# Performance work log

Measured on AMD Instinct MI355X. Metric: run time of the kernel, lower is better.

## Reference

```python
import jax, jax.numpy as jnp
import numpy as np
from functools import partial

WIDTH = 2560
LRU = 2560
HEADS = 8
DCONV = 4
B = 4
L = 2048


def setup_inputs() -> dict:
    key = jax.random.key(0)
    ks = jax.random.split(key, 16)
    bw = LRU // HEADS
    x = jax.random.normal(ks[0], (B, L, WIDTH), dtype=jnp.float32)
    segment_pos = jnp.broadcast_to(jnp.arange(L, dtype=jnp.int32), (B, L))
    # indices of the last DCONV frames of the left-padded conv input (length L+DCONV-1)
    base = (jnp.arange(DCONV, dtype=jnp.int32) + (L - 1))
    conv_idx = jnp.broadcast_to(base, (B, LRU, DCONV))
    s = 0.02
    return {
        "x": x,
        "segment_pos": segment_pos,
        "conv_idx": conv_idx,
        "Wx": jax.random.normal(ks[1], (LRU, WIDTH), jnp.float32) * s,
        "bx": jax.random.normal(ks[2], (LRU,), jnp.float32) * s,
        "Wy": jax.random.normal(ks[3], (LRU, WIDTH), jnp.float32) * s,
        "conv_w": jax.random.normal(ks[4], (LRU, DCONV), jnp.float32) * s,  # depthwise kernel
        "conv_b": jax.random.normal(ks[5], (LRU,), jnp.float32) * s,
        "gx_w": jax.random.normal(ks[6], (HEADS, bw, bw), jnp.float32) * s,
        "gx_b": jax.random.normal(ks[7], (HEADS, bw), jnp.float32) * s,
        "ga_w": jax.random.normal(ks[8], (HEADS, bw, bw), jnp.float32) * s,
        "ga_b": jax.random.normal(ks[9], (HEADS, bw), jnp.float32) * s,
        "a_param": jax.random.normal(ks[10], (LRU,), jnp.float32),
        "y_bias": jax.random.normal(ks[11], (1, 1, LRU), jnp.float32) * s,
        "Wout": jax.random.normal(ks[12], (WIDTH, LRU), jnp.float32) * s,
        "bout": jax.random.normal(ks[13], (WIDTH,), jnp.float32) * s,
    }


def _block_diag(x, w):
    # x: [B,L,(h*i)], w: [h,i,j] -> [B,L,(h*j)]
    b, l, _ = x.shape
    h, bw, _ = w.shape
    xb = x.reshape(b, l, h, bw)
    y = jnp.einsum('blhi,hij->blhj', xb, w)
    return y.reshape(b, l, h * bw)


def _scan_op(c1, c2):
    a1, b1 = c1
    a2, b2 = c2
    return (a1 * a2, a2 * b1 + b2)


def reference(x, segment_pos, conv_idx, Wx, bx, Wy, conv_w, conv_b,
              gx_w, gx_b, ga_w, ga_b, a_param, y_bias, Wout, bout):
    dc = conv_w.shape[1]
    seqlen = x.shape[1]

    y = jnp.einsum('bld,ed->ble', x, Wy)                 # linear_y (no bias)
    xl = jnp.einsum('bld,ed->ble', x, Wx) + bx           # linear_x

    # causal depthwise conv1d, padding dc-1 on the left, keep first seqlen
    xpad = jnp.pad(xl, ((0, 0), (dc - 1, 0), (0, 0)))    # [B, L+dc-1, LRU]
    xc = conv_b + sum(conv_w[:, k] * xpad[:, k:k + seqlen, :] for k in range(dc))

    # conv_state: gather of padded (channels-first) input at conv_idx
    conv_state = jnp.take_along_axis(xpad.transpose(0, 2, 1), conv_idx.astype(jnp.int32), axis=2)

    gx = _block_diag(xc, gx_w)  # fuse_bias=True: bias added inside rg_lru
    ga = _block_diag(xc, ga_w)

    # rg_lru_ref
    reset = (segment_pos == 0).astype(x.dtype)[..., None]        # [B,L,1]
    gate_x = jax.nn.sigmoid(gx + gx_b.reshape(-1))
    gate_a = jax.nn.sigmoid(ga + ga_b.reshape(-1))
    c = -8.0 * jax.nn.softplus(a_param)
    log_a = c * gate_a
    a = jnp.exp(log_a) * (1.0 - reset)
    multiplier = jnp.sqrt(1.0 - jnp.exp(2.0 * log_a))
    multiplier = reset + (1.0 - reset) * multiplier
    normalized_x = xc * gate_x * multiplier

    _, h = jax.lax.associative_scan(_scan_op, (a, normalized_x), axis=1)
    last_h = h[:, -1]

    out = h * jax.nn.gelu(y + y_bias, approximate=False)
    out = jnp.einsum('ble,de->bld', out, Wout) + bout    # linear_out
    return out, conv_state, last_h
```

## Files before the change

kernel.cpp:

```cpp
#include <hip/hip_runtime.h>
#include <hip/hip_bf16.h>

#define WIDTH_ 2560
#define LRU_   2560
#define HEADS_ 8
#define BW_    320
#define DCONV_ 4
#define BB     4
#define LL     2048
#define MROWS  (BB*LL)
#define NCH    32
#define CLEN   (LL/NCH)

typedef unsigned short ushort_t;
typedef __attribute__((ext_vector_type(8))) short short8;
typedef __attribute__((ext_vector_type(4))) float f32x4;

__device__ __forceinline__ unsigned short f2bf(float f) {
  union { float f; unsigned u; } v; v.f = f;
  unsigned r = v.u + 0x7fffu + ((v.u >> 16) & 1u);
  return (unsigned short)(r >> 16);
}
__device__ __forceinline__ float bf2f(unsigned short h) {
  union { unsigned u; float f; } v; v.u = ((unsigned)h) << 16;
  return v.f;
}
__device__ __forceinline__ void async_load16(const void* g, void* l) {
  __builtin_amdgcn_global_load_lds(
      (const __attribute__((address_space(1))) unsigned*)g,
      (__attribute__((address_space(3))) unsigned*)l, 16, 0, 0);
}
__device__ __forceinline__ float sigmoidf_(float x) {
  return 1.f / (1.f + __expf(-x));
}
__device__ __forceinline__ size_t pkaddr(int e, int m, int PL) {
  return ((size_t)(e >> 3) * PL + m) * 8 + (e & 7);
}

__global__ void tp_pack(const float* __restrict__ src, ushort_t* __restrict__ dst,
                        int R, int C, int PL, int RO) {
  __shared__ float tile[64][65];
  const int r0 = blockIdx.x * 64, c0 = blockIdx.y * 64;
  const int t = threadIdx.x;
#pragma unroll
  for (int it = 0; it < 4; ++it) {
    int row = it * 16 + (t >> 4);
    int col = (t & 15) * 4;
    *(float4*)&tile[row][col] = *(const float4*)&src[(size_t)(r0 + row) * C + c0 + col];
  }
  __syncthreads();
#pragma unroll
  for (int it = 0; it < 2; ++it) {
    int c8 = it * 4 + (t >> 6);
    int m  = t & 63;
    ushort_t o[8];
#pragma unroll
    for (int j = 0; j < 8; ++j) o[j] = f2bf(tile[m][c8 * 8 + j]);
    *(short8*)&dst[((size_t)(c0 / 8 + c8) * PL + RO + r0 + m) * 8] = *(short8*)o;
  }
}

__global__ void gw_pack2(const float* __restrict__ gxw, const float* __restrict__ gaw,
                         ushort_t* __restrict__ dst, int n_) {
  int i = blockIdx.x * blockDim.x + threadIdx.x;
  if (i >= 2 * n_) return;
  const float* w = (i < n_) ? gxw : gaw;
  int RO = (i < n_) ? 0 : BW_;
  int j = (i < n_) ? i : i - n_;
  int n = j % BW_;
  int k = (j / BW_) % BW_;
  int h = j / (BW_ * BW_);
  dst[((size_t)(h * 40 + (k >> 3)) * 640 + RO + n) * 8 + (k & 7)] =
      f2bf(w[((size_t)h * BW_ + k) * BW_ + n]);
}

__global__ void ctab_kernel(const float* __restrict__ apar, float* __restrict__ ctab) {
  int e = blockIdx.x * blockDim.x + threadIdx.x;
  if (e >= LRU_) return;
  float ap = apar[e];
  float sp = (ap > 15.f) ? ap : log1pf(expf(ap));
  ctab[e] = -8.f * sp;
}


#define STG_A(KT, H, BUF) do { \
  _Pragma("unroll") for (int u_ = 0; u_ < 2; ++u_) \
    async_load16(Ach + aoff[u_] + (size_t)(KT) * aKt + (H) * 2048, \
                 smem + ((BUF) * 2 + (H)) * 16384 + ldst[u_]); } while (0)
#define STG_B(KT, PART, BUF) do { \
  _Pragma("unroll") for (int u_ = (PART) ? 2 : 0; u_ < ((PART) ? NF : 2); ++u_) \
    async_load16(Bch + boff[u_] + (size_t)(KT) * bKt, \
                 smem + 65536 + (BUF) * BREG + bldst[u_]); } while (0)

#define PHASE(BUF, Q, STAGE_STMT, VMN) do { \
  __builtin_amdgcn_sched_barrier(0); \
  const char* Ah_ = smem + ((BUF) * 2 + wr) * 16384; \
  const char* Bh_ = smem + 65536 + (BUF) * BREG; \
  if ((Q) == 0) { \
    _Pragma("unroll") for (int nf = 0; nf < NF; ++nf) \
      _Pragma("unroll") for (int s = 0; s < 2; ++s) \
        bfr[nf][s] = *(const short8*)(Bh_ + (((s * 4 + l4) * BN) + wc * (BN / 4) + nf * 16 + l15) * 16); \
  } \
  short8 a_[2][2]; \
  _Pragma("unroll") for (int mm = 0; mm < 2; ++mm) \
    _Pragma("unroll") for (int s = 0; s < 2; ++s) \
      a_[mm][s] = *(const short8*)(Ah_ + ((s * 4 + l4) * 128 + ((Q) * 2 + mm) * 16 + l15) * 16); \
  STAGE_STMT; \
  __builtin_amdgcn_sched_barrier(0); \
  __builtin_amdgcn_s_barrier(); \
  asm volatile("s_waitcnt lgkmcnt(0)" ::: "memory"); \
  __builtin_amdgcn_sched_barrier(0); \
  __builtin_amdgcn_s_setprio(1); \
  _Pragma("unroll") for (int mm = 0; mm < 2; ++mm) \
    _Pragma("unroll") for (int nf = 0; nf < NF; ++nf) \
      _Pragma("unroll") for (int s = 0; s < 2; ++s) \
        acc[(Q) * 2 + mm][nf] = __builtin_amdgcn_mfma_f32_16x16x32_bf16( \
            a_[mm][s], bfr[nf][s], acc[(Q) * 2 + mm][nf], 0, 0, 0); \
  __builtin_amdgcn_s_setprio(0); \
  if ((VMN) == 5)      asm volatile("s_waitcnt vmcnt(5)" ::: "memory"); \
  else if ((VMN) == 4) asm volatile("s_waitcnt vmcnt(4)" ::: "memory"); \
  else if ((VMN) == 0) asm volatile("s_waitcnt vmcnt(0)" ::: "memory"); \
  __builtin_amdgcn_sched_barrier(0); \
  __builtin_amdgcn_s_barrier(); \
} while (0)

template<int EPI, int BN>
__global__ __launch_bounds__(512, 2)
void gemm_pk(const ushort_t* __restrict__ A,
             const ushort_t* __restrict__ B, int NPL,
             void* __restrict__ C0, void* __restrict__ C1,
             const float* __restrict__ bias) {
  constexpr int NF = BN / 64;
  constexpr int BREG = BN * 128;
  __shared__ char smem[65536 + 2 * BREG];
  const int tid = threadIdx.x;
  const int lane = tid & 63, w = tid >> 6;
  const int wr = w >> 2, wc = w & 3;
  const int l15 = lane & 15, l4 = lane >> 4;

  const int nblk = gridDim.x;
  const int TN = nblk >> 5;
  const int x8 = blockIdx.x & 7, c = blockIdx.x >> 3;
  const int tm = (x8 * 4 + c / TN) * 256;
  const int tn = (c % TN) * BN;

  const char* Ach = (const char*)A;
  const char* Bch = (const char*)B;
  const size_t aKt = (size_t)8 * MROWS * 16;
  const size_t bKt = (size_t)8 * NPL * 16;

  size_t aoff[2]; int ldst[2];
#pragma unroll
  for (int u = 0; u < 2; ++u) {
    int lb = (u * 512 + tid) * 16;
    int slot = lb >> 11, m = (lb >> 4) & 127;
    aoff[u] = ((size_t)slot * MROWS + tm + m) * 16;
    ldst[u] = lb;
  }
  size_t boff[NF]; int bldst[NF];
#pragma unroll
  for (int u = 0; u < NF; ++u) {
    int lb = (u * 512 + tid) * 16;
    int slot = lb / (BN * 16), n = (lb - slot * (BN * 16)) >> 4;
    boff[u] = ((size_t)slot * NPL + tn + n) * 16;
    bldst[u] = lb;
  }

  f32x4 acc[8][NF] = {};
  short8 bfr[NF][2];

  STG_B(0, 0, 0); STG_B(0, 1, 0);
  STG_A(0, 0, 0); STG_A(0, 1, 0);
  STG_B(1, 0, 1); STG_B(1, 1, 1);
  if (NF == 5) asm volatile("s_waitcnt vmcnt(5)" ::: "memory");
  else         asm volatile("s_waitcnt vmcnt(4)" ::: "memory");
  __builtin_amdgcn_sched_barrier(0);
  __builtin_amdgcn_s_barrier();

#pragma unroll 1
  for (int i = 0; i < 20; ++i) {
    const int k1 = 2 * i + 1, k2 = 2 * i + 2, k3 = 2 * i + 3;
    const bool v2 = (k2 < 40), v3 = (k3 < 40);
    PHASE(0, 0, STG_A(k1, 0, 1), -1);
    PHASE(0, 1, STG_A(k1, 1, 1), -1);
    PHASE(0, 2, if (v2) STG_B(k2, 0, 0), -1);
    PHASE(0, 3, if (v2) STG_B(k2, 1, 0), (v2 ? NF : 0));
    PHASE(1, 0, if (v2) STG_A(k2, 0, 0), -1);
    PHASE(1, 1, if (v2) STG_A(k2, 1, 0), -1);
    PHASE(1, 2, if (v3) STG_B(k3, 0, 1), -1);
    PHASE(1, 3, if (v3) STG_B(k3, 1, 1), (v3 ? NF : (v2 ? 0 : -1)));
  }

  const int crow0 = tm + wr * 128 + l4 * 4;
  const int ccol0 = tn + wc * (BN / 4) + l15;
#pragma unroll
  for (int m = 0; m < 8; ++m)
#pragma unroll
    for (int n = 0; n < NF; ++n) {
      const int col = ccol0 + n * 16;
#pragma unroll
      for (int r = 0; r < 4; ++r) {
        const int row = crow0 + m * 16 + r;
        float v = acc[m][n][r];
        if (EPI == 0) {
          ((float*)C0)[(size_t)row * 2560 + col] = v + bias[col];
        } else {
          if (col < 2560)
            ((ushort_t*)C0)[pkaddr(col, row, MROWS)] = f2bf(v + bias[col]);
          else
            ((ushort_t*)C1)[pkaddr(col - 2560, row, MROWS)] = f2bf(v);
        }
      }
    }
}

__global__ __launch_bounds__(256, 2)
void gate_gemm(const ushort_t* __restrict__ A,
               const ushort_t* __restrict__ Bw,
               ushort_t* __restrict__ GX,
               ushort_t* __restrict__ AAo,
               const float* __restrict__ gxb, const float* __restrict__ gab,
               const float* __restrict__ ctab, const int* __restrict__ seg) {
  constexpr int BM = 128, NF = 2;
  __shared__ char smem[24576];
  const int tid = threadIdx.x;
  const int w = tid >> 6, lane = tid & 63;
  const int wr = w >> 1, wc = w & 1;
  const int l15 = lane & 15, l4 = lane >> 4;

  const int bid = blockIdx.x;
  const int x8 = bid & 7;
  const int s = bid >> 3;
  const int member = s % 10;
  const int g = (s / 10) * 8 + x8;
  const int tm = (g & 63) * BM;
  const int z = g >> 6;
  const int tn = member * 64;

  const char* aS[2]; int lda_[2];
#pragma unroll
  for (int u = 0; u < 2; ++u) {
    int lb = (u * 256 + tid) * 16;
    int slot = lb >> 11, m = (lb >> 4) & 127;
    aS[u] = (const char*)A + ((size_t)(z * 40 + slot) * MROWS + tm + m) * 16;
    lda_[u] = lb;
  }
  const char* bS; int ldb_;
  {
    int lb = tid * 16;
    int slot = lb >> 10, n = (lb >> 4) & 63;
    bS = (const char*)Bw + ((size_t)(z * 40 + slot) * 640 + tn + n) * 16;
    ldb_ = 8192 + lb;
  }
  const size_t aStep = (size_t)4 * MROWS * 16;
  const size_t bStep = (size_t)4 * 640 * 16;

#define GSTG(KT, BUF) do { \
  _Pragma("unroll") for (int u_ = 0; u_ < 2; ++u_) \
    async_load16(aS[u_] + (size_t)(KT) * aStep, smem + (BUF) * 12288 + lda_[u_]); \
  async_load16(bS + (size_t)(KT) * bStep, smem + (BUF) * 12288 + ldb_); \
} while (0)

  f32x4 acc[4][NF] = {};
  const int aRd = l4 * 2048 + (wr * 64 + l15) * 16;
  const int bRd = 8192 + l4 * 1024 + (wc * 32 + l15) * 16;

  GSTG(0, 0);
#pragma unroll 1
  for (int kt = 0; kt < 10; ++kt) {
    const int p = kt & 1;
    if (kt < 9) {
      GSTG(kt + 1, p ^ 1);
      asm volatile("s_waitcnt vmcnt(3)" ::: "memory");
    } else {
      asm volatile("s_waitcnt vmcnt(0)" ::: "memory");
    }
    __builtin_amdgcn_sched_barrier(0);
    __builtin_amdgcn_s_barrier();
    const char* buf = smem + p * 12288;
    short8 af[4], bfr[NF];
#pragma unroll
    for (int mf = 0; mf < 4; ++mf)
      af[mf] = *(const short8*)(buf + aRd + mf * 256);
#pragma unroll
    for (int nf = 0; nf < NF; ++nf)
      bfr[nf] = *(const short8*)(buf + bRd + nf * 256);
#pragma unroll
    for (int mf = 0; mf < 4; ++mf)
#pragma unroll
      for (int nf = 0; nf < NF; ++nf)
        acc[mf][nf] = __builtin_amdgcn_mfma_f32_16x16x32_bf16(af[mf], bfr[nf], acc[mf][nf], 0, 0, 0);
    __builtin_amdgcn_sched_barrier(0);
    __builtin_amdgcn_s_barrier();
  }
#undef GSTG

  const int crow0 = tm + wr * 64 + l4 * 4;
  const int ccol0 = tn + wc * 32 + l15;
#pragma unroll
  for (int mf = 0; mf < 4; ++mf) {
#pragma unroll
    for (int nf = 0; nf < NF; ++nf) {
      const int cih = ccol0 + nf * 16;
#pragma unroll
      for (int r = 0; r < 4; ++r) {
        const int row = crow0 + mf * 16 + r;
        if (cih < BW_) {
          const int gc = z * BW_ + cih;
          float v = acc[mf][nf][r] + gxb[gc];
          float xc = bf2f(A[pkaddr(gc, row, MROWS)]);
          GX[pkaddr(gc, row, MROWS)] = f2bf(xc * sigmoidf_(v));
        } else {
          const int gc = z * BW_ + cih - BW_;
          float v = acc[mf][nf][r] + gab[gc];
          float la = ctab[gc] * sigmoidf_(v);
          float av = (seg[row] == 0) ? 0.f : expf(la);
          AAo[pkaddr(gc, row, MROWS)] = f2bf(av);
        }
      }
    }
  }
}

__global__ void conv_pk(const ushort_t* __restrict__ xl, const float* __restrict__ convw,
                        const float* __restrict__ convb, ushort_t* __restrict__ xc) {
  int i = blockIdx.x * blockDim.x + threadIdx.x;
  if (i >= 320 * MROWS) return;
  int m = i % MROWS;
  int p = i / MROWS;
  int t = m % LL;
  const ushort_t* pl = xl + (size_t)p * MROWS * 8;
  short8 v0 = {}, v1 = {}, v2 = {}, v3;
  v3 = *(const short8*)(pl + (size_t)m * 8);
  if (t >= 1) v2 = *(const short8*)(pl + (size_t)(m - 1) * 8);
  if (t >= 2) v1 = *(const short8*)(pl + (size_t)(m - 2) * 8);
  if (t >= 3) v0 = *(const short8*)(pl + (size_t)(m - 3) * 8);
  ushort_t o[8];
#pragma unroll
  for (int u = 0; u < 8; ++u) {
    int e = p * 8 + u;
    float4 wv = ((const float4*)convw)[e];
    float acc = convb[e];
    acc += wv.x * bf2f((ushort_t)v0[u]);
    acc += wv.y * bf2f((ushort_t)v1[u]);
    acc += wv.z * bf2f((ushort_t)v2[u]);
    acc += wv.w * bf2f((ushort_t)v3[u]);
    o[u] = f2bf(acc);
  }
  *(short8*)(xc + (size_t)p * MROWS * 8 + (size_t)m * 8) = *(short8*)o;
}

__global__ void conv_state_kernel(const ushort_t* __restrict__ xl, const int* __restrict__ cidx,
                                  float* __restrict__ cs) {
  int i = blockIdx.x * blockDim.x + threadIdx.x;
  if (i >= BB * LRU_ * DCONV_) return;
  int e = (i / DCONV_) % LRU_;
  int b = i / (DCONV_ * LRU_);
  int idx = cidx[i];
  int ts = idx - (DCONV_ - 1);
  float v = 0.f;
  if (ts >= 0 && ts < LL) v = bf2f(xl[pkaddr(e, b * LL + ts, MROWS)]);
  cs[i] = v;
}

__global__ void scanA(const ushort_t* __restrict__ AA, const ushort_t* __restrict__ GX,
                      float* __restrict__ cA, float* __restrict__ cH) {
  int i = blockIdx.x * blockDim.x + threadIdx.x;
  if (i >= BB * NCH * LRU_) return;
  int e = i % LRU_;
  int c = (i / LRU_) % NCH;
  int b = i / (LRU_ * NCH);
  float Ap = 1.f, h = 0.f;
  size_t base = pkaddr(e, b * LL + c * CLEN, MROWS);
  for (int t = 0; t < CLEN; ++t) {
    size_t j = base + (size_t)t * 8;
    float a = bf2f(AA[j]);
    float nx = bf2f(GX[j]) * sqrtf(fmaxf(0.f, 1.f - a * a));
    Ap *= a;
    h = a * h + nx;
  }
  cA[i] = Ap; cH[i] = h;
}

__global__ void scanB(const float* __restrict__ cA, const float* __restrict__ cH,
                      float* __restrict__ hInit) {
  int i = blockIdx.x * blockDim.x + threadIdx.x;
  if (i >= BB * LRU_) return;
  int e = i % LRU_;
  int b = i / LRU_;
  float h = 0.f;
  for (int c = 0; c < NCH; ++c) {
    size_t j = ((size_t)b * NCH + c) * LRU_ + e;
    hInit[j] = h;
    h = cA[j] * h + cH[j];
  }
}

__global__ void scanC(const ushort_t* __restrict__ AA, const ushort_t* __restrict__ GXpre,
                      const float* __restrict__ hInit, const ushort_t* __restrict__ ybf,
                      const float* __restrict__ ybias, float* __restrict__ lastH) {
  int i = blockIdx.x * blockDim.x + threadIdx.x;
  if (i >= BB * NCH * LRU_) return;
  int e = i % LRU_;
  int c = (i / LRU_) % NCH;
  int b = i / (LRU_ * NCH);
  float h = hInit[i];
  float yb = ybias[e];
  ushort_t* pre = (ushort_t*)GXpre;
  size_t base = pkaddr(e, b * LL + c * CLEN, MROWS);
  for (int t = 0; t < CLEN; ++t) {
    size_t j = base + (size_t)t * 8;
    float a = bf2f(AA[j]);
    float nx = bf2f(GXpre[j]) * sqrtf(fmaxf(0.f, 1.f - a * a));
    h = a * h + nx;
    float yv = bf2f(ybf[j]) + yb;
    float g = 0.5f * yv * (1.f + erff(yv * 0.70710678118f));
    pre[j] = f2bf(h * g);
  }
  if (c == NCH - 1) lastH[(size_t)b * LRU_ + e] = h;
}

extern "C" void kernel_launch(void* const* d_in, const int* in_sizes, int n_in,
                              void* d_out, int out_size, void* d_ws, size_t ws_size,
                              hipStream_t stream) {
  const float* x     = (const float*)d_in[0];
  const int*   seg   = (const int*)d_in[1];
  const int*   cidx  = (const int*)d_in[2];
  const float* Wx    = (const float*)d_in[3];
  const float* bx    = (const float*)d_in[4];
  const float* Wy    = (const float*)d_in[5];
  const float* convw = (const float*)d_in[6];
  const float* convb = (const float*)d_in[7];
  const float* gxw   = (const float*)d_in[8];
  const float* gxb   = (const float*)d_in[9];
  const float* gaw   = (const float*)d_in[10];
  const float* gab   = (const float*)d_in[11];
  const float* apar  = (const float*)d_in[12];
  const float* ybias = (const float*)d_in[13];
  const float* Wout  = (const float*)d_in[14];
  const float* bout  = (const float*)d_in[15];

  float* out    = (float*)d_out;
  float* cs_out = out + (size_t)MROWS * WIDTH_;
  float* lh_out = cs_out + (size_t)BB * LRU_ * DCONV_;

  ushort_t* ybf = (ushort_t*)d_out;
  ushort_t* AA  = (ushort_t*)((char*)d_out + (size_t)41943040);

  const size_t SZ_BIG = (size_t)MROWS * LRU_ * 2;
  const size_t SZ_WC  = (size_t)(2 * LRU_) * WIDTH_ * 2;
  const size_t SZ_GW  = (size_t)HEADS_ * 640 * BW_ * 2;
  const size_t SZ_SM  = (size_t)BB * NCH * LRU_ * 4;
  size_t need = SZ_BIG * 3 + SZ_WC + SZ_GW + 10240 + SZ_SM * 3;
  if (ws_size < need) return;

  char* p = (char*)d_ws;
  ushort_t* xpk   = (ushort_t*)p; p += SZ_BIG;
  ushort_t* wpk   = (ushort_t*)p; p += SZ_WC;
  ushort_t* T2    = (ushort_t*)p; p += SZ_BIG;
  ushort_t* xcbf  = (ushort_t*)p; p += SZ_BIG;
  ushort_t* gwT   = (ushort_t*)p; p += SZ_GW;
  float*    ctab  = (float*)p;    p += 10240;
  float*    cA    = (float*)p;    p += SZ_SM;
  float*    cH    = (float*)p;    p += SZ_SM;
  float*    hInit = (float*)p;    p += SZ_SM;
  ushort_t* woutpk = wpk;

  const int BLK = 256;
  tp_pack<<<dim3(MROWS / 64, WIDTH_ / 64), 256, 0, stream>>>(x, xpk, MROWS, WIDTH_, MROWS, 0);
  tp_pack<<<dim3(LRU_ / 64, WIDTH_ / 64), 256, 0, stream>>>(Wx, wpk, LRU_, WIDTH_, 2 * LRU_, 0);
  tp_pack<<<dim3(LRU_ / 64, WIDTH_ / 64), 256, 0, stream>>>(Wy, wpk, LRU_, WIDTH_, 2 * LRU_, LRU_);

  gemm_pk<1, 256><<<640, 512, 0, stream>>>(xpk, wpk, 2 * LRU_, T2, ybf, bx);

  tp_pack<<<dim3(LRU_ / 64, WIDTH_ / 64), 256, 0, stream>>>(Wout, woutpk, WIDTH_, LRU_, WIDTH_, 0);

  conv_pk<<<(320 * MROWS + BLK - 1) / BLK, BLK, 0, stream>>>(T2, convw, convb, xcbf);
  conv_state_kernel<<<(BB * LRU_ * DCONV_ + BLK - 1) / BLK, BLK, 0, stream>>>(T2, cidx, cs_out);

  gw_pack2<<<(2 * HEADS_ * BW_ * BW_ + BLK - 1) / BLK, BLK, 0, stream>>>(gxw, gaw, gwT, HEADS_ * BW_ * BW_);
  ctab_kernel<<<(LRU_ + BLK - 1) / BLK, BLK, 0, stream>>>(apar, ctab);

  gate_gemm<<<5120, BLK, 0, stream>>>(
      xcbf, gwT, T2, AA, gxb, gab, ctab, seg);

  scanA<<<(BB * NCH * LRU_ + BLK - 1) / BLK, BLK, 0, stream>>>(AA, T2, cA, cH);
  scanB<<<(BB * LRU_ + BLK - 1) / BLK, BLK, 0, stream>>>(cA, cH, hInit);
  scanC<<<(BB * NCH * LRU_ + BLK - 1) / BLK, BLK, 0, stream>>>(AA, T2, hInit, ybf, ybias, lh_out);

  gemm_pk<0, 320><<<256, 512, 0, stream>>>(T2, woutpk, WIDTH_, out, nullptr, bout);
}
```

Measured before the change: 553.3 us.

## Restructure gate GEMM to keep A tile resident and merge small launches

```diff
diff --git a/kernel.cpp b/kernel.cpp
--- a/kernel.cpp
+++ b/kernel.cpp
@@ -37,16 +37,19 @@
   return ((size_t)(e >> 3) * PL + m) * 8 + (e & 7);
 }
 
-__global__ void tp_pack(const float* __restrict__ src, ushort_t* __restrict__ dst,
-                        int R, int C, int PL, int RO) {
+__global__ void tp_pack(const float* __restrict__ src, const float* __restrict__ src2,
+                        ushort_t* __restrict__ dst, int R, int C, int PL, int RO) {
   __shared__ float tile[64][65];
+  const int z = blockIdx.z;
+  const float* s = (z == 0) ? src : src2;
+  const int ro = RO + z * R;
   const int r0 = blockIdx.x * 64, c0 = blockIdx.y * 64;
   const int t = threadIdx.x;
 #pragma unroll
   for (int it = 0; it < 4; ++it) {
     int row = it * 16 + (t >> 4);
     int col = (t & 15) * 4;
-    *(float4*)&tile[row][col] = *(const float4*)&src[(size_t)(r0 + row) * C + c0 + col];
+    *(float4*)&tile[row][col] = *(const float4*)&s[(size_t)(r0 + row) * C + c0 + col];
   }
   __syncthreads();
 #pragma unroll
@@ -56,32 +59,31 @@
     ushort_t o[8];
 #pragma unroll
     for (int j = 0; j < 8; ++j) o[j] = f2bf(tile[m][c8 * 8 + j]);
-    *(short8*)&dst[((size_t)(c0 / 8 + c8) * PL + RO + r0 + m) * 8] = *(short8*)o;
-  }
-}
-
-__global__ void gw_pack2(const float* __restrict__ gxw, const float* __restrict__ gaw,
-                         ushort_t* __restrict__ dst, int n_) {
+    *(short8*)&dst[((size_t)(c0 / 8 + c8) * PL + ro + r0 + m) * 8] = *(short8*)o;
+  }
+}
+
+__global__ void prep_kernel(const float* __restrict__ gxw, const float* __restrict__ gaw,
+                            ushort_t* __restrict__ dst,
+                            const float* __restrict__ apar, float* __restrict__ ctab) {
+  const int n_ = HEADS_ * BW_ * BW_;
   int i = blockIdx.x * blockDim.x + threadIdx.x;
-  if (i >= 2 * n_) return;
-  const float* w = (i < n_) ? gxw : gaw;
-  int RO = (i < n_) ? 0 : BW_;
-  int j = (i < n_) ? i : i - n_;
-  int n = j % BW_;
-  int k = (j / BW_) % BW_;
-  int h = j / (BW_ * BW_);
-  dst[((size_t)(h * 40 + (k >> 3)) * 640 + RO + n) * 8 + (k & 7)] =
-      f2bf(w[((size_t)h * BW_ + k) * BW_ + n]);
-}
-
-__global__ void ctab_kernel(const float* __restrict__ apar, float* __restrict__ ctab) {
-  int e = blockIdx.x * blockDim.x + threadIdx.x;
-  if (e >= LRU_) return;
-  float ap = apar[e];
-  float sp = (ap > 15.f) ? ap : log1pf(expf(ap));
-  ctab[e] = -8.f * sp;
-}
-
+  if (i < 2 * n_) {
+    const float* w = (i < n_) ? gxw : gaw;
+    int RO = (i < n_) ? 0 : BW_;
+    int j = (i < n_) ? i : i - n_;
+    int n = j % BW_;
+    int k = (j / BW_) % BW_;
+    int h = j / (BW_ * BW_);
+    dst[((size_t)(h * 40 + (k >> 3)) * 640 + RO + n) * 8 + (k & 7)] =
+        f2bf(w[((size_t)h * BW_ + k) * BW_ + n]);
+  } else if (i < 2 * n_ + LRU_) {
+    int e = i - 2 * n_;
+    float ap = apar[e];
+    float sp = (ap > 15.f) ? ap : log1pf(expf(ap));
+    ctab[e] = -8.f * sp;
+  }
+}
 
 #define STG_A(KT, H, BUF) do { \
   _Pragma("unroll") for (int u_ = 0; u_ < 2; ++u_) \
@@ -221,146 +223,131 @@
                ushort_t* __restrict__ AAo,
                const float* __restrict__ gxb, const float* __restrict__ gab,
                const float* __restrict__ ctab, const int* __restrict__ seg) {
-  constexpr int BM = 128, NF = 2;
-  __shared__ char smem[24576];
+  __shared__ char smem[81920];
   const int tid = threadIdx.x;
-  const int w = tid >> 6, lane = tid & 63;
-  const int wr = w >> 1, wc = w & 1;
+  const int lane = tid & 63, w = tid >> 6;
   const int l15 = lane & 15, l4 = lane >> 4;
 
   const int bid = blockIdx.x;
-  const int x8 = bid & 7;
-  const int s = bid >> 3;
-  const int member = s % 10;
-  const int g = (s / 10) * 8 + x8;
-  const int tm = (g & 63) * BM;
-  const int z = g >> 6;
-  const int tn = member * 64;
-
-  const char* aS[2]; int lda_[2];
-#pragma unroll
-  for (int u = 0; u < 2; ++u) {
+  const int x8 = bid & 7, s0 = bid >> 3;
+  const int z = s0 >> 4;
+  const int tm = ((s0 & 15) * 8 + x8) * 64;
+
+#pragma unroll
+  for (int u = 0; u < 10; ++u) {
     int lb = (u * 256 + tid) * 16;
-    int slot = lb >> 11, m = (lb >> 4) & 127;
-    aS[u] = (const char*)A + ((size_t)(z * 40 + slot) * MROWS + tm + m) * 16;
-    lda_[u] = lb;
-  }
-  const char* bS; int ldb_;
-  {
-    int lb = tid * 16;
-    int slot = lb >> 10, n = (lb >> 4) & 63;
-    bS = (const char*)Bw + ((size_t)(z * 40 + slot) * 640 + tn + n) * 16;
-    ldb_ = 8192 + lb;
-  }
-  const size_t aStep = (size_t)4 * MROWS * 16;
-  const size_t bStep = (size_t)4 * 640 * 16;
-
-#define GSTG(KT, BUF) do { \
-  _Pragma("unroll") for (int u_ = 0; u_ < 2; ++u_) \
-    async_load16(aS[u_] + (size_t)(KT) * aStep, smem + (BUF) * 12288 + lda_[u_]); \
-  async_load16(bS + (size_t)(KT) * bStep, smem + (BUF) * 12288 + ldb_); \
-} while (0)
-
-  f32x4 acc[4][NF] = {};
-  const int aRd = l4 * 2048 + (wr * 64 + l15) * 16;
-  const int bRd = 8192 + l4 * 1024 + (wc * 32 + l15) * 16;
-
-  GSTG(0, 0);
+    int slot = lb >> 10, m = (lb >> 4) & 63;
+    async_load16((const char*)A + ((size_t)(z * 40 + slot) * MROWS + tm + m) * 16,
+                 smem + lb);
+  }
+#define GSTG_B(S, BUF) do { \
+  _Pragma("unroll") for (int u_ = 0; u_ < 5; ++u_) { \
+    int lb_ = (u_ * 256 + tid) * 16; \
+    int slot_ = lb_ >> 9, n_ = (lb_ >> 4) & 31; \
+    async_load16((const char*)Bw + ((size_t)(z * 40 + slot_) * 640 + (S) * 32 + n_) * 16, \
+                 smem + 40960 + (BUF) * 20480 + lb_); \
+  } } while (0)
+
+  GSTG_B(0, 0);
+  asm volatile("s_waitcnt vmcnt(0)" ::: "memory");
+  __builtin_amdgcn_sched_barrier(0);
+  __builtin_amdgcn_s_barrier();
+
+  short8 af[10];
+#pragma unroll
+  for (int kk = 0; kk < 10; ++kk)
+    af[kk] = *(const short8*)(smem + (((kk * 4 + l4) * 64) + w * 16 + l15) * 16);
+
 #pragma unroll 1
-  for (int kt = 0; kt < 10; ++kt) {
-    const int p = kt & 1;
-    if (kt < 9) {
-      GSTG(kt + 1, p ^ 1);
-      asm volatile("s_waitcnt vmcnt(3)" ::: "memory");
+  for (int s = 0; s < 20; ++s) {
+    const int p = s & 1;
+    if (s < 19) {
+      GSTG_B(s + 1, p ^ 1);
+      asm volatile("s_waitcnt vmcnt(5)" ::: "memory");
     } else {
       asm volatile("s_waitcnt vmcnt(0)" ::: "memory");
     }
     __builtin_amdgcn_sched_barrier(0);
     __builtin_amdgcn_s_barrier();
-    const char* buf = smem + p * 12288;
-    short8 af[4], bfr[NF];
-#pragma unroll
-    for (int mf = 0; mf < 4; ++mf)
-      af[mf] = *(const short8*)(buf + aRd + mf * 256);
-#pragma unroll
-    for (int nf = 0; nf < NF; ++nf)
-      bfr[nf] = *(const short8*)(buf + bRd + nf * 256);
-#pragma unroll
-    for (int mf = 0; mf < 4; ++mf)
-#pragma unroll
-      for (int nf = 0; nf < NF; ++nf)
-        acc[mf][nf] = __builtin_amdgcn_mfma_f32_16x16x32_bf16(af[mf], bfr[nf], acc[mf][nf], 0, 0, 0);
-    __builtin_amdgcn_sched_barrier(0);
-    __builtin_amdgcn_s_barrier();
-  }
-#undef GSTG
-
-  const int crow0 = tm + wr * 64 + l4 * 4;
-  const int ccol0 = tn + wc * 32 + l15;
-#pragma unroll
-  for (int mf = 0; mf < 4; ++mf) {
-#pragma unroll
-    for (int nf = 0; nf < NF; ++nf) {
-      const int cih = ccol0 + nf * 16;
+
+    const char* Bb = smem + 40960 + p * 20480;
+    f32x4 acc[2] = {};
+#pragma unroll
+    for (int kk = 0; kk < 10; ++kk) {
+#pragma unroll
+      for (int nf = 0; nf < 2; ++nf) {
+        short8 bfr = *(const short8*)(Bb + (((kk * 4 + l4) * 32) + nf * 16 + l15) * 16);
+        acc[nf] = __builtin_amdgcn_mfma_f32_16x16x32_bf16(af[kk], bfr, acc[nf], 0, 0, 0);
+      }
+    }
+
+    const bool isGX = (s < 10);
+    const int cbase = (isGX ? s : s - 10) * 32;
+#pragma unroll
+    for (int nf = 0; nf < 2; ++nf) {
+      const int cin = nf * 16 + l15;
+      const int ch = cbase + cin;
+      const int gc = z * BW_ + ch;
 #pragma unroll
       for (int r = 0; r < 4; ++r) {
-        const int row = crow0 + mf * 16 + r;
-        if (cih < BW_) {
-          const int gc = z * BW_ + cih;
-          float v = acc[mf][nf][r] + gxb[gc];
-          float xc = bf2f(A[pkaddr(gc, row, MROWS)]);
+        const int lrow = w * 16 + l4 * 4 + r;
+        const int row = tm + lrow;
+        if (isGX) {
+          float v = acc[nf][r] + gxb[gc];
+          float xc = bf2f(*(const ushort_t*)(smem + (((ch >> 3) * 64) + lrow) * 16 + (ch & 7) * 2));
           GX[pkaddr(gc, row, MROWS)] = f2bf(xc * sigmoidf_(v));
         } else {
-          const int gc = z * BW_ + cih - BW_;
-          float v = acc[mf][nf][r] + gab[gc];
+          float v = acc[nf][r] + gab[gc];
           float la = ctab[gc] * sigmoidf_(v);
           float av = (seg[row] == 0) ? 0.f : expf(la);
           AAo[pkaddr(gc, row, MROWS)] = f2bf(av);
         }
       }
     }
-  }
+    __builtin_amdgcn_sched_barrier(0);
+    __builtin_amdgcn_s_barrier();
+  }
+#undef GSTG_B
 }
 
 __global__ void conv_pk(const ushort_t* __restrict__ xl, const float* __restrict__ convw,
-                        const float* __restrict__ convb, ushort_t* __restrict__ xc) {
+                        const float* __restrict__ convb, ushort_t* __restrict__ xc,
+                        const int* __restrict__ cidx, float* __restrict__ cs) {
   int i = blockIdx.x * blockDim.x + threadIdx.x;
-  if (i >= 320 * MROWS) return;
-  int m = i % MROWS;
-  int p = i / MROWS;
-  int t = m % LL;
-  const ushort_t* pl = xl + (size_t)p * MROWS * 8;
-  short8 v0 = {}, v1 = {}, v2 = {}, v3;
-  v3 = *(const short8*)(pl + (size_t)m * 8);
-  if (t >= 1) v2 = *(const short8*)(pl + (size_t)(m - 1) * 8);
-  if (t >= 2) v1 = *(const short8*)(pl + (size_t)(m - 2) * 8);
-  if (t >= 3) v0 = *(const short8*)(pl + (size_t)(m - 3) * 8);
-  ushort_t o[8];
-#pragma unroll
-  for (int u = 0; u < 8; ++u) {
-    int e = p * 8 + u;
-    float4 wv = ((const float4*)convw)[e];
-    float acc = convb[e];
-    acc += wv.x * bf2f((ushort_t)v0[u]);
-    acc += wv.y * bf2f((ushort_t)v1[u]);
-    acc += wv.z * bf2f((ushort_t)v2[u]);
-    acc += wv.w * bf2f((ushort_t)v3[u]);
-    o[u] = f2bf(acc);
-  }
-  *(short8*)(xc + (size_t)p * MROWS * 8 + (size_t)m * 8) = *(short8*)o;
-}
-
-__global__ void conv_state_kernel(const ushort_t* __restrict__ xl, const int* __restrict__ cidx,
-                                  float* __restrict__ cs) {
-  int i = blockIdx.x * blockDim.x + threadIdx.x;
-  if (i >= BB * LRU_ * DCONV_) return;
-  int e = (i / DCONV_) % LRU_;
-  int b = i / (DCONV_ * LRU_);
-  int idx = cidx[i];
-  int ts = idx - (DCONV_ - 1);
-  float v = 0.f;
-  if (ts >= 0 && ts < LL) v = bf2f(xl[pkaddr(e, b * LL + ts, MROWS)]);
-  cs[i] = v;
+  if (i < 320 * MROWS) {
+    int m = i % MROWS;
+    int p = i / MROWS;
+    int t = m % LL;
+    const ushort_t* pl = xl + (size_t)p * MROWS * 8;
+    short8 v0 = {}, v1 = {}, v2 = {}, v3;
+    v3 = *(const short8*)(pl + (size_t)m * 8);
+    if (t >= 1) v2 = *(const short8*)(pl + (size_t)(m - 1) * 8);
+    if (t >= 2) v1 = *(const short8*)(pl + (size_t)(m - 2) * 8);
+    if (t >= 3) v0 = *(const short8*)(pl + (size_t)(m - 3) * 8);
+    ushort_t o[8];
+#pragma unroll
+    for (int u = 0; u < 8; ++u) {
+      int e = p * 8 + u;
+      float4 wv = ((const float4*)convw)[e];
+      float acc = convb[e];
+      acc += wv.x * bf2f((ushort_t)v0[u]);
+      acc += wv.y * bf2f((ushort_t)v1[u]);
+      acc += wv.z * bf2f((ushort_t)v2[u]);
+      acc += wv.w * bf2f((ushort_t)v3[u]);
+      o[u] = f2bf(acc);
+    }
+    *(short8*)(xc + (size_t)p * MROWS * 8 + (size_t)m * 8) = *(short8*)o;
+  } else {
+    int j = i - 320 * MROWS;
+    if (j >= BB * LRU_ * DCONV_) return;
+    int e = (j / DCONV_) % LRU_;
+    int b = j / (DCONV_ * LRU_);
+    int idx = cidx[j];
+    int ts = idx - (DCONV_ - 1);
+    float v = 0.f;
+    if (ts >= 0 && ts < LL) v = bf2f(xl[pkaddr(e, b * LL + ts, MROWS)]);
+    cs[j] = v;
+  }
 }
 
 __global__ void scanA(const ushort_t* __restrict__ AA, const ushort_t* __restrict__ GX,
@@ -467,22 +454,20 @@
   ushort_t* woutpk = wpk;
 
   const int BLK = 256;
-  tp_pack<<<dim3(MROWS / 64, WIDTH_ / 64), 256, 0, stream>>>(x, xpk, MROWS, WIDTH_, MROWS, 0);
-  tp_pack<<<dim3(LRU_ / 64, WIDTH_ / 64), 256, 0, stream>>>(Wx, wpk, LRU_, WIDTH_, 2 * LRU_, 0);
-  tp_pack<<<dim3(LRU_ / 64, WIDTH_ / 64), 256, 0, stream>>>(Wy, wpk, LRU_, WIDTH_, 2 * LRU_, LRU_);
+  tp_pack<<<dim3(MROWS / 64, WIDTH_ / 64, 1), 256, 0, stream>>>(x, nullptr, xpk, MROWS, WIDTH_, MROWS, 0);
+  tp_pack<<<dim3(LRU_ / 64, WIDTH_ / 64, 2), 256, 0, stream>>>(Wx, Wy, wpk, LRU_, WIDTH_, 2 * LRU_, 0);
 
   gemm_pk<1, 256><<<640, 512, 0, stream>>>(xpk, wpk, 2 * LRU_, T2, ybf, bx);
 
-  tp_pack<<<dim3(LRU_ / 64, WIDTH_ / 64), 256, 0, stream>>>(Wout, woutpk, WIDTH_, LRU_, WIDTH_, 0);
-
-  conv_pk<<<(320 * MROWS + BLK - 1) / BLK, BLK, 0, stream>>>(T2, convw, convb, xcbf);
-  conv_state_kernel<<<(BB * LRU_ * DCONV_ + BLK - 1) / BLK, BLK, 0, stream>>>(T2, cidx, cs_out);
-
-  gw_pack2<<<(2 * HEADS_ * BW_ * BW_ + BLK - 1) / BLK, BLK, 0, stream>>>(gxw, gaw, gwT, HEADS_ * BW_ * BW_);
-  ctab_kernel<<<(LRU_ + BLK - 1) / BLK, BLK, 0, stream>>>(apar, ctab);
-
-  gate_gemm<<<5120, BLK, 0, stream>>>(
-      xcbf, gwT, T2, AA, gxb, gab, ctab, seg);
+  tp_pack<<<dim3(LRU_ / 64, WIDTH_ / 64, 1), 256, 0, stream>>>(Wout, nullptr, woutpk, WIDTH_, LRU_, WIDTH_, 0);
+
+  conv_pk<<<(320 * MROWS + BB * LRU_ * DCONV_ + BLK - 1) / BLK, BLK, 0, stream>>>(
+      T2, convw, convb, xcbf, cidx, cs_out);
+
+  prep_kernel<<<(2 * HEADS_ * BW_ * BW_ + LRU_ + BLK - 1) / BLK, BLK, 0, stream>>>(
+      gxw, gaw, gwT, apar, ctab);
+
+  gate_gemm<<<1024, BLK, 0, stream>>>(xcbf, gwT, T2, AA, gxb, gab, ctab, seg);
 
   scanA<<<(BB * NCH * LRU_ + BLK - 1) / BLK, BLK, 0, stream>>>(AA, T2, cA, cH);
   scanB<<<(BB * LRU_ + BLK - 1) / BLK, BLK, 0, stream>>>(cA, cH, hInit);
```

Result: slower. 594.1 us (+7.4%).
